# Kernel optimization log

Hardware: AMD Instinct MI355X
Metric: run time of the kernel (lower is better)

## Reference

```python
import jax, jax.numpy as jnp
import numpy as np

H = 50  # hidden_size


def _lstm_layer(x, W_ih, W_hh, b_ih, b_hh):
    """Single LSTM layer, batch_first input x: [B, T, D] -> [B, T, H].
    PyTorch gate order in the 4H dim: i, f, g, o."""
    B, T, D = x.shape
    # Precompute input projections for all timesteps: [T, B, 4H]
    x_proj = jnp.einsum('btd,gd->tbg', x, W_ih) + (b_ih + b_hh)

    def step(carry, xt):
        h, c = carry
        gates = xt + h @ W_hh.T  # [B, 4H]
        i, f, g, o = jnp.split(gates, 4, axis=-1)
        i = jax.nn.sigmoid(i)
        f = jax.nn.sigmoid(f)
        g = jnp.tanh(g)
        o = jax.nn.sigmoid(o)
        c = f * c + i * g
        h = o * jnp.tanh(c)
        return (h, c), h

    h0 = jnp.zeros((B, H), dtype=x.dtype)
    c0 = jnp.zeros((B, H), dtype=x.dtype)
    _, hs = jax.lax.scan(step, (h0, c0), x_proj)  # hs: [T, B, H]
    return jnp.transpose(hs, (1, 0, 2))  # [B, T, H]


def setup_inputs() -> dict:
    key = jax.random.key(0)
    ks = jax.random.split(key, 11)
    B, T = 2048, 512
    s = 1.0 / np.sqrt(H)  # PyTorch uniform init bound
    u = lambda k, shape: jax.random.uniform(k, shape, jnp.float32, -s, s)
    return {
        'x': jax.random.normal(ks[0], (B, T, 1), dtype=jnp.float32),
        'W_ih0': u(ks[1], (4 * H, 1)),
        'W_hh0': u(ks[2], (4 * H, H)),
        'b_ih0': u(ks[3], (4 * H,)),
        'b_hh0': u(ks[4], (4 * H,)),
        'W_ih1': u(ks[5], (4 * H, H)),
        'W_hh1': u(ks[6], (4 * H, H)),
        'b_ih1': u(ks[7], (4 * H,)),
        'b_hh1': u(ks[8], (4 * H,)),
        'W_fc': u(ks[9], (1, H)),
        'b_fc': u(ks[10], (1,)),
    }


def reference(x, W_ih0, W_hh0, b_ih0, b_hh0, W_ih1, W_hh1, b_ih1, b_hh1, W_fc, b_fc):
    out = _lstm_layer(x, W_ih0, W_hh0, b_ih0, b_hh0)     # [B, T, H]
    out = _lstm_layer(out, W_ih1, W_hh1, b_ih1, b_hh1)   # [B, T, H]
    return out[:, -1, :] @ W_fc.T + b_fc                  # [B, 1]
```

## Files before the change

### kernel.cpp

```cpp
#include <hip/hip_runtime.h>

#define TT   512
#define HH   50
#define MB   8
#define NW   13
#define NTHR (NW * 64)

typedef _Float16 f16x8 __attribute__((ext_vector_type(8)));
typedef float    f32x4 __attribute__((ext_vector_type(4)));

#define L2E 1.4426950408889634f

__device__ __forceinline__ float rcp_f(float v) { return __builtin_amdgcn_rcpf(v); }
__device__ __forceinline__ float ex2_f(float v) { return __builtin_amdgcn_exp2f(v); }

__global__ __launch_bounds__(NTHR, 1)
void lstm2_kernel(const float* __restrict__ x,
                  const float* __restrict__ W_ih0, const float* __restrict__ W_hh0,
                  const float* __restrict__ b_ih0, const float* __restrict__ b_hh0,
                  const float* __restrict__ W_ih1, const float* __restrict__ W_hh1,
                  const float* __restrict__ b_ih1, const float* __restrict__ b_hh1,
                  const float* __restrict__ W_fc,  const float* __restrict__ b_fc,
                  float* __restrict__ out)
{
    __shared__ __align__(16) _Float16 sh0[2][2][4][16][8];
    __shared__ __align__(16) _Float16 sh1[2][2][4][16][8];
    __shared__ float sh_x[MB][TT + 4];
    __shared__ float shf[MB][52];
    __shared__ float sh_wfc[HH];

    const int tid = threadIdx.x;
    const int w   = tid >> 6;
    const int l   = tid & 63;
    const int q   = l >> 4;
    const int n   = l & 15;
    const int b0  = blockIdx.x * MB;

    for (int i = tid; i < 2 * 2 * 4 * 16 * 8; i += NTHR) {
        (&sh0[0][0][0][0][0])[i] = (_Float16)0.0f;
        (&sh1[0][0][0][0][0])[i] = (_Float16)0.0f;
    }
    for (int i = tid; i < MB * TT; i += NTHR)
        sh_x[i >> 9][i & (TT - 1)] = x[(size_t)b0 * TT + i];
    for (int i = tid; i < HH; i += NTHR) sh_wfc[i] = W_fc[i];

    const int  u_r   = w * 4 + (n >> 2);
    const bool rowok = (u_r < HH);
    const int  grow  = (n & 3) * HH + (rowok ? u_r : 0);
    const float srow = ((n & 3) == 2) ? (2.0f * L2E) : (-L2E);

    f16x8 whh0[2], wih1[2], whh1[2];
    #pragma unroll
    for (int ki = 0; ki < 2; ++ki) {
        #pragma unroll
        for (int e = 0; e < 8; ++e) {
            int k = ki * 32 + q * 8 + e;
            bool ok = rowok && (k < HH);
            whh0[ki][e] = ok ? (_Float16)(srow * W_hh0[grow * HH + k]) : (_Float16)0.0f;
            wih1[ki][e] = ok ? (_Float16)(srow * W_ih1[grow * HH + k]) : (_Float16)0.0f;
            whh1[ki][e] = ok ? (_Float16)(srow * W_hh1[grow * HH + k]) : (_Float16)0.0f;
        }
    }

    const bool isL1 = (n >= 8);
    const int  u    = 4 * w + q;
    const int  cb   = n & 7;
    const bool wr   = (u < HH);
    const int  uc   = wr ? u : 0;

    float bza[4], wza[4];
    #pragma unroll
    for (int e = 0; e < 4; ++e) {
        int gr = e * HH + uc;
        float sc = (e == 2) ? (2.0f * L2E) : (-L2E);
        bza[e] = sc * (isL1 ? (b_ih1[gr] + b_hh1[gr]) : (b_ih0[gr] + b_hh0[gr]));
        wza[e] = isL1 ? 0.0f : (sc * W_ih0[gr]);
    }

    const int uk = uc >> 5, uq2 = (uc >> 3) & 3, ue = uc & 7;
    _Float16* wpA0 = isL1 ? &sh1[1][uk][uq2][cb + 8][ue] : &sh0[1][uk][uq2][cb][ue];
    _Float16* wpA1 = isL1 ? &sh1[0][uk][uq2][cb + 8][ue] : &sh0[0][uk][uq2][cb][ue];

    const float* xq = &sh_x[cb][0];
    const f32x4 z = {0.0f, 0.0f, 0.0f, 0.0f};
    float cst = 0.0f;

    __syncthreads();

#define MFMA(A, B, C) __builtin_amdgcn_mfma_f32_16x16x32_f16((A), (B), (C), 0, 0, 0)

#define STEP(P, T0, XI)                                                           \
    {                                                                             \
        f16x8 hb0 = *(const f16x8*)&sh0[P][0][q][n][0];                           \
        f16x8 hb1 = *(const f16x8*)&sh0[P][1][q][n][0];                           \
        f16x8 pb0 = *(const f16x8*)&sh1[P][0][q][n][0];                           \
        f16x8 pb1 = *(const f16x8*)&sh1[P][1][q][n][0];                           \
        f32x4 a0 = MFMA(whh0[0], hb0, z);                                         \
        a0 = MFMA(whh0[1], hb1, a0);                                              \
        f32x4 a1 = MFMA(wih1[0], hb0, z);                                         \
        a1 = MFMA(wih1[1], hb1, a1);                                              \
        a1 = MFMA(whh1[0], pb0, a1);                                              \
        a1 = MFMA(whh1[1], pb1, a1);                                              \
        float xi = (XI);                                                          \
        float g0 = (isL1 ? a1[0] : a0[0]) + bza[0];                               \
        float g1 = (isL1 ? a1[1] : a0[1]) + bza[1];                               \
        float g2 = (isL1 ? a1[2] : a0[2]) + bza[2];                               \
        float g3 = (isL1 ? a1[3] : a0[3]) + bza[3];                               \
        g0 = __builtin_fmaf(xi, wza[0], g0);                                      \
        g1 = __builtin_fmaf(xi, wza[1], g1);                                      \
        g2 = __builtin_fmaf(xi, wza[2], g2);                                      \
        g3 = __builtin_fmaf(xi, wza[3], g3);                                      \
        float eI = ex2_f(g0), eF = ex2_f(g1), tG = ex2_f(g2), eO = ex2_f(g3);     \
        float dI = 1.0f + eI, dF = 1.0f + eF, dO = 1.0f + eO;                     \
        float IG = (tG - 1.0f) * rcp_f(dI * (tG + 1.0f));                         \
        float cn = __builtin_fmaf(rcp_f(dF), cst, IG);                            \
        cst = ((T0) && isL1) ? 0.0f : cn;                                         \
        float cc = fminf(fmaxf(cst, -16.0f), 16.0f);                              \
        float tc = ex2_f(cc * (2.0f * L2E));                                      \
        float hv = (tc - 1.0f) * rcp_f(dO * (tc + 1.0f));                         \
        if (wr && !((T0) && isL1)) {                                              \
            _Float16 h16 = (_Float16)hv;                                          \
            _Float16* wp = (P) ? wpA1 : wpA0;                                     \
            wp[0] = h16;                                                          \
            if (!isL1) wp[64] = h16;                     \
        }                                                                         \
        __syncthreads();                                                          \
    }

    STEP(0, 1, xq[0])
    for (int k2 = 0; k2 < 255; ++k2) {
        STEP(1, 0, xq[1])
        STEP(0, 0, xq[2])
        xq += 2;
    }
    STEP(1, 0, xq[1])
#undef STEP

    {
        f16x8 hb0 = *(const f16x8*)&sh0[0][0][q][n][0];
        f16x8 hb1 = *(const f16x8*)&sh0[0][1][q][n][0];
        f16x8 pb0 = *(const f16x8*)&sh1[0][0][q][n][0];
        f16x8 pb1 = *(const f16x8*)&sh1[0][1][q][n][0];
        f32x4 a1 = MFMA(wih1[0], hb0, z);
        a1 = MFMA(wih1[1], hb1, a1);
        a1 = MFMA(whh1[0], pb0, a1);
        a1 = MFMA(whh1[1], pb1, a1);
        if (isL1 && wr) {
            float g0 = a1[0] + bza[0];
            float g1 = a1[1] + bza[1];
            float g2 = a1[2] + bza[2];
            float g3 = a1[3] + bza[3];
            float eI = ex2_f(g0), eF = ex2_f(g1), tG = ex2_f(g2), eO = ex2_f(g3);
            float dI = 1.0f + eI, dF = 1.0f + eF, dO = 1.0f + eO;
            float IG = (tG - 1.0f) * rcp_f(dI * (tG + 1.0f));
            float cn = __builtin_fmaf(rcp_f(dF), cst, IG);
            float cc = fminf(fmaxf(cn, -16.0f), 16.0f);
            float tc = ex2_f(cc * (2.0f * L2E));
            shf[cb][uc] = (tc - 1.0f) * rcp_f(dO * (tc + 1.0f));
        }
    }
    __syncthreads();

    if (tid < MB) {
        float s = b_fc[0];
        for (int j = 0; j < HH; ++j) s += shf[tid][j] * sh_wfc[j];
        out[b0 + tid] = s;
    }
#undef MFMA
}

extern "C" void kernel_launch(void* const* d_in, const int* in_sizes, int n_in,
                              void* d_out, int out_size, void* d_ws, size_t ws_size,
                              hipStream_t stream) {
    const float* xin   = (const float*)d_in[0];
    const float* W_ih0 = (const float*)d_in[1];
    const float* W_hh0 = (const float*)d_in[2];
    const float* b_ih0 = (const float*)d_in[3];
    const float* b_hh0 = (const float*)d_in[4];
    const float* W_ih1 = (const float*)d_in[5];
    const float* W_hh1 = (const float*)d_in[6];
    const float* b_ih1 = (const float*)d_in[7];
    const float* b_hh1 = (const float*)d_in[8];
    const float* W_fc  = (const float*)d_in[9];
    const float* b_fc  = (const float*)d_in[10];
    float* out = (float*)d_out;

    lstm2_kernel<<<dim3(2048 / MB), dim3(NTHR), 0, stream>>>(
        xin, W_ih0, W_hh0, b_ih0, b_hh0, W_ih1, W_hh1, b_ih1, b_hh1, W_fc, b_fc, out);
}
```

Before: 258.3 us.

## Fold input projection and biases into MFMA via augmented hidden-state columns

Appends the scalar input x_t and a constant 1 as extra K columns of the layer-0 hidden buffer, with the corresponding weight columns holding W_ih0 and the biases. The per-step bias adds and input FMAs therefore disappear from the gate computation. One lane copies the next x value into the shared buffer each step, and x is stored as fp16. Layer-1's two MFMA chains are split into independent accumulators to shorten the dependency chain. The trade-off is lower precision, since x and the biases are now rounded to fp16.

```diff
diff --git a/kernel.cpp b/kernel.cpp
--- a/kernel.cpp
+++ b/kernel.cpp
@@ -25,7 +25,7 @@
 {
     __shared__ __align__(16) _Float16 sh0[2][2][4][16][8];
     __shared__ __align__(16) _Float16 sh1[2][2][4][16][8];
-    __shared__ float sh_x[MB][TT + 4];
+    __shared__ _Float16 sh_xh[MB][TT + 8];
     __shared__ float shf[MB][52];
     __shared__ float sh_wfc[HH];
 
@@ -41,8 +41,13 @@
         (&sh1[0][0][0][0][0])[i] = (_Float16)0.0f;
     }
     for (int i = tid; i < MB * TT; i += NTHR)
-        sh_x[i >> 9][i & (TT - 1)] = x[(size_t)b0 * TT + i];
+        sh_xh[i >> 9][i & (TT - 1)] = (_Float16)x[(size_t)b0 * TT + i];
+    for (int i = tid; i < MB * 8; i += NTHR)
+        sh_xh[i >> 3][TT + (i & 7)] = (_Float16)0.0f;
     for (int i = tid; i < HH; i += NTHR) sh_wfc[i] = W_fc[i];
+    __syncthreads();
+    if (tid < 32) sh0[tid >> 4][1][2][tid & 15][3] = (_Float16)1.0f;
+    if (tid < MB) sh0[0][1][2][tid][2] = (_Float16)x[(size_t)(b0 + tid) * TT];
 
     const int  u_r   = w * 4 + (n >> 2);
     const bool rowok = (u_r < HH);
@@ -55,10 +60,22 @@
         #pragma unroll
         for (int e = 0; e < 8; ++e) {
             int k = ki * 32 + q * 8 + e;
-            bool ok = rowok && (k < HH);
-            whh0[ki][e] = ok ? (_Float16)(srow * W_hh0[grow * HH + k]) : (_Float16)0.0f;
-            wih1[ki][e] = ok ? (_Float16)(srow * W_ih1[grow * HH + k]) : (_Float16)0.0f;
-            whh1[ki][e] = ok ? (_Float16)(srow * W_hh1[grow * HH + k]) : (_Float16)0.0f;
+            float a0v = 0.0f, a1v = 0.0f, a2v = 0.0f;
+            if (rowok) {
+                if (k < HH) {
+                    a0v = W_hh0[grow * HH + k];
+                    a1v = W_ih1[grow * HH + k];
+                    a2v = W_hh1[grow * HH + k];
+                } else if (k == HH) {
+                    a0v = W_ih0[grow];
+                } else if (k == HH + 1) {
+                    a0v = b_ih0[grow] + b_hh0[grow];
+                    a1v = b_ih1[grow] + b_hh1[grow];
+                }
+            }
+            whh0[ki][e] = (_Float16)(srow * a0v);
+            wih1[ki][e] = (_Float16)(srow * a1v);
+            whh1[ki][e] = (_Float16)(srow * a2v);
         }
     }
 
@@ -68,28 +85,21 @@
     const bool wr   = (u < HH);
     const int  uc   = wr ? u : 0;
 
-    float bza[4], wza[4];
-    #pragma unroll
-    for (int e = 0; e < 4; ++e) {
-        int gr = e * HH + uc;
-        float sc = (e == 2) ? (2.0f * L2E) : (-L2E);
-        bza[e] = sc * (isL1 ? (b_ih1[gr] + b_hh1[gr]) : (b_ih0[gr] + b_hh0[gr]));
-        wza[e] = isL1 ? 0.0f : (sc * W_ih0[gr]);
-    }
+    const bool wrel = (w == 12) && (q == 2) && (n < 8);
 
     const int uk = uc >> 5, uq2 = (uc >> 3) & 3, ue = uc & 7;
     _Float16* wpA0 = isL1 ? &sh1[1][uk][uq2][cb + 8][ue] : &sh0[1][uk][uq2][cb][ue];
     _Float16* wpA1 = isL1 ? &sh1[0][uk][uq2][cb + 8][ue] : &sh0[0][uk][uq2][cb][ue];
 
-    const float* xq = &sh_x[cb][0];
     const f32x4 z = {0.0f, 0.0f, 0.0f, 0.0f};
     float cst = 0.0f;
+    int   xt  = 1;
 
     __syncthreads();
 
 #define MFMA(A, B, C) __builtin_amdgcn_mfma_f32_16x16x32_f16((A), (B), (C), 0, 0, 0)
 
-#define STEP(P, T0, XI)                                                           \
+#define STEP(P, T0)                                                               \
     {                                                                             \
         f16x8 hb0 = *(const f16x8*)&sh0[P][0][q][n][0];                           \
         f16x8 hb1 = *(const f16x8*)&sh0[P][1][q][n][0];                           \
@@ -99,17 +109,15 @@
         a0 = MFMA(whh0[1], hb1, a0);                                              \
         f32x4 a1 = MFMA(wih1[0], hb0, z);                                         \
         a1 = MFMA(wih1[1], hb1, a1);                                              \
-        a1 = MFMA(whh1[0], pb0, a1);                                              \
-        a1 = MFMA(whh1[1], pb1, a1);                                              \
-        float xi = (XI);                                                          \
-        float g0 = (isL1 ? a1[0] : a0[0]) + bza[0];                               \
-        float g1 = (isL1 ? a1[1] : a0[1]) + bza[1];                               \
-        float g2 = (isL1 ? a1[2] : a0[2]) + bza[2];                               \
-        float g3 = (isL1 ? a1[3] : a0[3]) + bza[3];                               \
-        g0 = __builtin_fmaf(xi, wza[0], g0);                                      \
-        g1 = __builtin_fmaf(xi, wza[1], g1);                                      \
-        g2 = __builtin_fmaf(xi, wza[2], g2);                                      \
-        g3 = __builtin_fmaf(xi, wza[3], g3);                                      \
+        f32x4 a2 = MFMA(whh1[0], pb0, z);                                         \
+        a2 = MFMA(whh1[1], pb1, a2);                                              \
+        a1 += a2;                                                                 \
+        if (wrel) sh0[(P) ^ 1][1][2][n][2] = sh_xh[n][xt];                        \
+        ++xt;                                                                     \
+        float g0 = isL1 ? a1[0] : a0[0];                                          \
+        float g1 = isL1 ? a1[1] : a0[1];                                          \
+        float g2 = isL1 ? a1[2] : a0[2];                                          \
+        float g3 = isL1 ? a1[3] : a0[3];                                          \
         float eI = ex2_f(g0), eF = ex2_f(g1), tG = ex2_f(g2), eO = ex2_f(g3);     \
         float dI = 1.0f + eI, dF = 1.0f + eF, dO = 1.0f + eO;                     \
         float IG = (tG - 1.0f) * rcp_f(dI * (tG + 1.0f));                         \
@@ -127,13 +135,12 @@
         __syncthreads();                                                          \
     }
 
-    STEP(0, 1, xq[0])
+    STEP(0, 1)
     for (int k2 = 0; k2 < 255; ++k2) {
-        STEP(1, 0, xq[1])
-        STEP(0, 0, xq[2])
-        xq += 2;
+        STEP(1, 0)
+        STEP(0, 0)
     }
-    STEP(1, 0, xq[1])
+    STEP(1, 0)
 #undef STEP
 
     {
@@ -146,11 +153,8 @@
         a1 = MFMA(whh1[0], pb0, a1);
         a1 = MFMA(whh1[1], pb1, a1);
         if (isL1 && wr) {
-            float g0 = a1[0] + bza[0];
-            float g1 = a1[1] + bza[1];
-            float g2 = a1[2] + bza[2];
-            float g3 = a1[3] + bza[3];
-            float eI = ex2_f(g0), eF = ex2_f(g1), tG = ex2_f(g2), eO = ex2_f(g3);
+            float eI = ex2_f(a1[0]), eF = ex2_f(a1[1]);
+            float tG = ex2_f(a1[2]), eO = ex2_f(a1[3]);
             float dI = 1.0f + eI, dF = 1.0f + eF, dO = 1.0f + eO;
             float IG = (tG - 1.0f) * rcp_f(dI * (tG + 1.0f));
             float cn = __builtin_fmaf(rcp_f(dF), cst, IG);
```

Result: slower. 282.2 us (+9.3%).

## Split warps into layer-0 and layer-1 groups with two-phase overlapped schedule

Applied to the files above, without the earlier changes.

Restructures the recurrence so 7 warps own layer 0 and 7 own layer 1. Each timestep is split into two barrier-separated phases, so one group's MFMAs overlap with the other group's gate math. Each warp now handles two row tiles with its own weights, instead of every warp computing both layers with half its lanes idle in the gate math. This adds a second __syncthreads per timestep and raises the warp count to 14. It also changes the fp16 h buffer layout for layer 1.

```diff
diff --git a/kernel.cpp b/kernel.cpp
--- a/kernel.cpp
+++ b/kernel.cpp
@@ -3,7 +3,7 @@
 #define TT   512
 #define HH   50
 #define MB   8
-#define NW   13
+#define NW   14
 #define NTHR (NW * 64)
 
 typedef _Float16 f16x8 __attribute__((ext_vector_type(8)));
@@ -13,6 +13,18 @@
 
 __device__ __forceinline__ float rcp_f(float v) { return __builtin_amdgcn_rcpf(v); }
 __device__ __forceinline__ float ex2_f(float v) { return __builtin_amdgcn_exp2f(v); }
+
+__device__ __forceinline__ float lstm_chain(float g0, float g1, float g2, float g3,
+                                            float& cst) {
+    float eI = ex2_f(g0), eF = ex2_f(g1), tG = ex2_f(g2), eO = ex2_f(g3);
+    float dI = 1.0f + eI, dF = 1.0f + eF, dO = 1.0f + eO;
+    float IG = (tG - 1.0f) * rcp_f(dI * (tG + 1.0f));
+    float cn = __builtin_fmaf(rcp_f(dF), cst, IG);
+    cst = cn;
+    float cc = fminf(fmaxf(cn, -16.0f), 16.0f);
+    float tc = ex2_f(cc * (2.0f * L2E));
+    return (tc - 1.0f) * rcp_f(dO * (tc + 1.0f));
+}
 
 __global__ __launch_bounds__(NTHR, 1)
 void lstm2_kernel(const float* __restrict__ x,
@@ -35,6 +47,8 @@
     const int q   = l >> 4;
     const int n   = l & 15;
     const int b0  = blockIdx.x * MB;
+    const bool isA = (w < 7);
+    const int  wg  = isA ? w : (w - 7);
 
     for (int i = tid; i < 2 * 2 * 4 * 16 * 8; i += NTHR) {
         (&sh0[0][0][0][0][0])[i] = (_Float16)0.0f;
@@ -44,120 +58,152 @@
         sh_x[i >> 9][i & (TT - 1)] = x[(size_t)b0 * TT + i];
     for (int i = tid; i < HH; i += NTHR) sh_wfc[i] = W_fc[i];
 
-    const int  u_r   = w * 4 + (n >> 2);
-    const bool rowok = (u_r < HH);
-    const int  grow  = (n & 3) * HH + (rowok ? u_r : 0);
     const float srow = ((n & 3) == 2) ? (2.0f * L2E) : (-L2E);
-
-    f16x8 whh0[2], wih1[2], whh1[2];
+    f16x8 wfA[2][2], wfB[2][2];
     #pragma unroll
-    for (int ki = 0; ki < 2; ++ki) {
+    for (int tt = 0; tt < 2; ++tt) {
+        int tile = 2 * wg + tt;
+        int ur   = 4 * tile + (n >> 2);
+        bool rok = (ur < HH);
+        int grow = (n & 3) * HH + (rok ? ur : 0);
         #pragma unroll
-        for (int e = 0; e < 8; ++e) {
-            int k = ki * 32 + q * 8 + e;
-            bool ok = rowok && (k < HH);
-            whh0[ki][e] = ok ? (_Float16)(srow * W_hh0[grow * HH + k]) : (_Float16)0.0f;
-            wih1[ki][e] = ok ? (_Float16)(srow * W_ih1[grow * HH + k]) : (_Float16)0.0f;
-            whh1[ki][e] = ok ? (_Float16)(srow * W_hh1[grow * HH + k]) : (_Float16)0.0f;
+        for (int ki = 0; ki < 2; ++ki) {
+            #pragma unroll
+            for (int e = 0; e < 8; ++e) {
+                int k = ki * 32 + q * 8 + e;
+                bool ok = rok && (k < HH);
+                float vA = 0.0f, vB = 0.0f;
+                if (ok) {
+                    if (isA) { vA = W_hh0[grow * HH + k]; }
+                    else     { vA = W_ih1[grow * HH + k]; vB = W_hh1[grow * HH + k]; }
+                }
+                wfA[tt][ki][e] = (_Float16)(srow * vA);
+                wfB[tt][ki][e] = (_Float16)(srow * vB);
+            }
         }
     }
 
-    const bool isL1 = (n >= 8);
-    const int  u    = 4 * w + q;
-    const int  cb   = n & 7;
-    const bool wr   = (u < HH);
-    const int  uc   = wr ? u : 0;
-
-    float bza[4], wza[4];
+    const int  u  = 8 * wg + ((n & 8) ? 4 : 0) + q;
+    const int  cb = n & 7;
+    const bool wr = (u < HH);
+    const int  uc = wr ? u : 0;
+
+    float bz[4], wz[4];
     #pragma unroll
     for (int e = 0; e < 4; ++e) {
         int gr = e * HH + uc;
         float sc = (e == 2) ? (2.0f * L2E) : (-L2E);
-        bza[e] = sc * (isL1 ? (b_ih1[gr] + b_hh1[gr]) : (b_ih0[gr] + b_hh0[gr]));
-        wza[e] = isL1 ? 0.0f : (sc * W_ih0[gr]);
+        bz[e] = sc * (isA ? (b_ih0[gr] + b_hh0[gr]) : (b_ih1[gr] + b_hh1[gr]));
+        wz[e] = isA ? (sc * W_ih0[gr]) : 0.0f;
     }
 
     const int uk = uc >> 5, uq2 = (uc >> 3) & 3, ue = uc & 7;
-    _Float16* wpA0 = isL1 ? &sh1[1][uk][uq2][cb + 8][ue] : &sh0[1][uk][uq2][cb][ue];
-    _Float16* wpA1 = isL1 ? &sh1[0][uk][uq2][cb + 8][ue] : &sh0[0][uk][uq2][cb][ue];
+    _Float16* wpP0 = isA ? &sh0[0][uk][uq2][cb][ue] : &sh1[0][uk][uq2][cb][ue];
+    _Float16* wpP1 = isA ? &sh0[1][uk][uq2][cb][ue] : &sh1[1][uk][uq2][cb][ue];
 
     const float* xq = &sh_x[cb][0];
     const f32x4 z = {0.0f, 0.0f, 0.0f, 0.0f};
+    f32x4 acc0 = z, acc1 = z;
     float cst = 0.0f;
 
     __syncthreads();
 
 #define MFMA(A, B, C) __builtin_amdgcn_mfma_f32_16x16x32_f16((A), (B), (C), 0, 0, 0)
 
-#define STEP(P, T0, XI)                                                           \
+#define PHASE1(P, BG)                                                             \
     {                                                                             \
-        f16x8 hb0 = *(const f16x8*)&sh0[P][0][q][n][0];                           \
-        f16x8 hb1 = *(const f16x8*)&sh0[P][1][q][n][0];                           \
-        f16x8 pb0 = *(const f16x8*)&sh1[P][0][q][n][0];                           \
-        f16x8 pb1 = *(const f16x8*)&sh1[P][1][q][n][0];                           \
-        f32x4 a0 = MFMA(whh0[0], hb0, z);                                         \
-        a0 = MFMA(whh0[1], hb1, a0);                                              \
-        f32x4 a1 = MFMA(wih1[0], hb0, z);                                         \
-        a1 = MFMA(wih1[1], hb1, a1);                                              \
-        a1 = MFMA(whh1[0], pb0, a1);                                              \
-        a1 = MFMA(whh1[1], pb1, a1);                                              \
-        float xi = (XI);                                                          \
-        float g0 = (isL1 ? a1[0] : a0[0]) + bza[0];                               \
-        float g1 = (isL1 ? a1[1] : a0[1]) + bza[1];                               \
-        float g2 = (isL1 ? a1[2] : a0[2]) + bza[2];                               \
-        float g3 = (isL1 ? a1[3] : a0[3]) + bza[3];                               \
-        g0 = __builtin_fmaf(xi, wza[0], g0);                                      \
-        g1 = __builtin_fmaf(xi, wza[1], g1);                                      \
-        g2 = __builtin_fmaf(xi, wza[2], g2);                                      \
-        g3 = __builtin_fmaf(xi, wza[3], g3);                                      \
-        float eI = ex2_f(g0), eF = ex2_f(g1), tG = ex2_f(g2), eO = ex2_f(g3);     \
-        float dI = 1.0f + eI, dF = 1.0f + eF, dO = 1.0f + eO;                     \
-        float IG = (tG - 1.0f) * rcp_f(dI * (tG + 1.0f));                         \
-        float cn = __builtin_fmaf(rcp_f(dF), cst, IG);                            \
-        cst = ((T0) && isL1) ? 0.0f : cn;                                         \
-        float cc = fminf(fmaxf(cst, -16.0f), 16.0f);                              \
-        float tc = ex2_f(cc * (2.0f * L2E));                                      \
-        float hv = (tc - 1.0f) * rcp_f(dO * (tc + 1.0f));                         \
-        if (wr && !((T0) && isL1)) {                                              \
-            _Float16 h16 = (_Float16)hv;                                          \
-            _Float16* wp = (P) ? wpA1 : wpA0;                                     \
-            wp[0] = h16;                                                          \
-            if (!isL1) wp[64] = h16;                     \
+        if (isA) {                                                                \
+            f16x8 hb0 = *(const f16x8*)&sh0[(P) ^ 1][0][q][n][0];                 \
+            f16x8 hb1 = *(const f16x8*)&sh0[(P) ^ 1][1][q][n][0];                 \
+            acc0 = MFMA(wfA[0][0], hb0, z);                                       \
+            acc0 = MFMA(wfA[0][1], hb1, acc0);                                    \
+            acc1 = MFMA(wfA[1][0], hb0, z);                                       \
+            acc1 = MFMA(wfA[1][1], hb1, acc1);                                    \
+        } else if (BG) {                                                          \
+            float g0 = ((n & 8) ? acc1[0] : acc0[0]) + bz[0];                     \
+            float g1 = ((n & 8) ? acc1[1] : acc0[1]) + bz[1];                     \
+            float g2 = ((n & 8) ? acc1[2] : acc0[2]) + bz[2];                     \
+            float g3 = ((n & 8) ? acc1[3] : acc0[3]) + bz[3];                     \
+            float hv = lstm_chain(g0, g1, g2, g3, cst);                           \
+            if (wr) {                                                             \
+                _Float16 h16 = (_Float16)hv;                                      \
+                _Float16* wp = (P) ? wpP1 : wpP0;                                 \
+                wp[0] = h16; wp[64] = h16;                                        \
+            }                                                                     \
         }                                                                         \
         __syncthreads();                                                          \
     }
 
-    STEP(0, 1, xq[0])
+#define PHASE2(P, XI)                                                             \
+    {                                                                             \
+        if (isA) {                                                                \
+            float xi = (XI);                                                      \
+            float g0 = __builtin_fmaf(xi, wz[0], ((n & 8) ? acc1[0] : acc0[0]) + bz[0]); \
+            float g1 = __builtin_fmaf(xi, wz[1], ((n & 8) ? acc1[1] : acc0[1]) + bz[1]); \
+            float g2 = __builtin_fmaf(xi, wz[2], ((n & 8) ? acc1[2] : acc0[2]) + bz[2]); \
+            float g3 = __builtin_fmaf(xi, wz[3], ((n & 8) ? acc1[3] : acc0[3]) + bz[3]); \
+            float hv = lstm_chain(g0, g1, g2, g3, cst);                           \
+            if (wr) {                                                             \
+                _Float16 h16 = (_Float16)hv;                                      \
+                _Float16* wp = (P) ? wpP1 : wpP0;                                 \
+                wp[0] = h16; wp[64] = h16;                                        \
+            }                                                                     \
+        } else {                                                                  \
+            f16x8 hb0 = *(const f16x8*)&sh0[(P) ^ 1][0][q][n][0];                 \
+            f16x8 hb1 = *(const f16x8*)&sh0[(P) ^ 1][1][q][n][0];                 \
+            f16x8 pb0 = *(const f16x8*)&sh1[P][0][q][n][0];                       \
+            f16x8 pb1 = *(const f16x8*)&sh1[P][1][q][n][0];                       \
+            acc0 = MFMA(wfA[0][0], hb0, z);                                       \
+            acc0 = MFMA(wfA[0][1], hb1, acc0);                                    \
+            acc0 = MFMA(wfB[0][0], pb0, acc0);                                    \
+            acc0 = MFMA(wfB[0][1], pb1, acc0);                                    \
+            acc1 = MFMA(wfA[1][0], hb0, z);                                       \
+            acc1 = MFMA(wfA[1][1], hb1, acc1);                                    \
+            acc1 = MFMA(wfB[1][0], pb0, acc1);                                    \
+            acc1 = MFMA(wfB[1][1], pb1, acc1);                                    \
+        }                                                                         \
+        __syncthreads();                                                          \
+    }
+
+    PHASE1(0, 0) PHASE2(0, xq[0])
+    PHASE1(1, 0) PHASE2(1, xq[1])
+
     for (int k2 = 0; k2 < 255; ++k2) {
-        STEP(1, 0, xq[1])
-        STEP(0, 0, xq[2])
+        PHASE1(0, 1) PHASE2(0, xq[2])
+        PHASE1(1, 1) PHASE2(1, xq[3])
         xq += 2;
     }
-    STEP(1, 0, xq[1])
-#undef STEP
-
-    {
-        f16x8 hb0 = *(const f16x8*)&sh0[0][0][q][n][0];
-        f16x8 hb1 = *(const f16x8*)&sh0[0][1][q][n][0];
+#undef PHASE1
+#undef PHASE2
+
+    if (!isA) {
+        float g0 = ((n & 8) ? acc1[0] : acc0[0]) + bz[0];
+        float g1 = ((n & 8) ? acc1[1] : acc0[1]) + bz[1];
+        float g2 = ((n & 8) ? acc1[2] : acc0[2]) + bz[2];
+        float g3 = ((n & 8) ? acc1[3] : acc0[3]) + bz[3];
+        float hv = lstm_chain(g0, g1, g2, g3, cst);
+        if (wr) { _Float16 h16 = (_Float16)hv; wpP0[0] = h16; wpP0[64] = h16; }
+    }
+    __syncthreads();
+    if (!isA) {
+        f16x8 hb0 = *(const f16x8*)&sh0[1][0][q][n][0];
+        f16x8 hb1 = *(const f16x8*)&sh0[1][1][q][n][0];
         f16x8 pb0 = *(const f16x8*)&sh1[0][0][q][n][0];
         f16x8 pb1 = *(const f16x8*)&sh1[0][1][q][n][0];
-        f32x4 a1 = MFMA(wih1[0], hb0, z);
-        a1 = MFMA(wih1[1], hb1, a1);
-        a1 = MFMA(whh1[0], pb0, a1);
-        a1 = MFMA(whh1[1], pb1, a1);
-        if (isL1 && wr) {
-            float g0 = a1[0] + bza[0];
-            float g1 = a1[1] + bza[1];
-            float g2 = a1[2] + bza[2];
-            float g3 = a1[3] + bza[3];
-            float eI = ex2_f(g0), eF = ex2_f(g1), tG = ex2_f(g2), eO = ex2_f(g3);
-            float dI = 1.0f + eI, dF = 1.0f + eF, dO = 1.0f + eO;
-            float IG = (tG - 1.0f) * rcp_f(dI * (tG + 1.0f));
-            float cn = __builtin_fmaf(rcp_f(dF), cst, IG);
-            float cc = fminf(fmaxf(cn, -16.0f), 16.0f);
-            float tc = ex2_f(cc * (2.0f * L2E));
-            shf[cb][uc] = (tc - 1.0f) * rcp_f(dO * (tc + 1.0f));
-        }
+        acc0 = MFMA(wfA[0][0], hb0, z);
+        acc0 = MFMA(wfA[0][1], hb1, acc0);
+        acc0 = MFMA(wfB[0][0], pb0, acc0);
+        acc0 = MFMA(wfB[0][1], pb1, acc0);
+        acc1 = MFMA(wfA[1][0], hb0, z);
+        acc1 = MFMA(wfA[1][1], hb1, acc1);
+        acc1 = MFMA(wfB[1][0], pb0, acc1);
+        acc1 = MFMA(wfB[1][1], pb1, acc1);
+        float g0 = ((n & 8) ? acc1[0] : acc0[0]) + bz[0];
+        float g1 = ((n & 8) ? acc1[1] : acc0[1]) + bz[1];
+        float g2 = ((n & 8) ? acc1[2] : acc0[2]) + bz[2];
+        float g3 = ((n & 8) ? acc1[3] : acc0[3]) + bz[3];
+        float hv = lstm_chain(g0, g1, g2, g3, cst);
+        if (wr) shf[cb][uc] = hv;
     }
     __syncthreads();
 
```

Result: slower. 320.3 us (+24.0%).

## Fuse both LSTM layers into one packed MFMA chain with bias in accumulator

Applied to the files above, without the earlier changes.

Packs W_hh0, W_ih1 and W_hh1 into one K=160 weight fragment so each step runs a single five-MFMA chain over a unified shared h buffer, instead of separate layer-0 and layer-1 chains. The bias and input-projection FMA are folded into the accumulator's initial value, and the clamp uses fmed3. This cuts total MFMA count and select logic per step. In exchange, the dependent MFMA chain for layer 0 gets longer and each step needs one more LDS read.

```diff
diff --git a/kernel.cpp b/kernel.cpp
--- a/kernel.cpp
+++ b/kernel.cpp
@@ -5,6 +5,7 @@
 #define MB   8
 #define NW   13
 #define NTHR (NW * 64)
+#define BUFH 2560
 
 typedef _Float16 f16x8 __attribute__((ext_vector_type(8)));
 typedef float    f32x4 __attribute__((ext_vector_type(4)));
@@ -23,8 +24,7 @@
                   const float* __restrict__ W_fc,  const float* __restrict__ b_fc,
                   float* __restrict__ out)
 {
-    __shared__ __align__(16) _Float16 sh0[2][2][4][16][8];
-    __shared__ __align__(16) _Float16 sh1[2][2][4][16][8];
+    __shared__ __align__(16) _Float16 shh[2][BUFH];
     __shared__ float sh_x[MB][TT + 4];
     __shared__ float shf[MB][52];
     __shared__ float sh_wfc[HH];
@@ -36,10 +36,7 @@
     const int n   = l & 15;
     const int b0  = blockIdx.x * MB;
 
-    for (int i = tid; i < 2 * 2 * 4 * 16 * 8; i += NTHR) {
-        (&sh0[0][0][0][0][0])[i] = (_Float16)0.0f;
-        (&sh1[0][0][0][0][0])[i] = (_Float16)0.0f;
-    }
+    for (int i = tid; i < 2 * BUFH; i += NTHR) (&shh[0][0])[i] = (_Float16)0.0f;
     for (int i = tid; i < MB * TT; i += NTHR)
         sh_x[i >> 9][i & (TT - 1)] = x[(size_t)b0 * TT + i];
     for (int i = tid; i < HH; i += NTHR) sh_wfc[i] = W_fc[i];
@@ -49,16 +46,19 @@
     const int  grow  = (n & 3) * HH + (rowok ? u_r : 0);
     const float srow = ((n & 3) == 2) ? (2.0f * L2E) : (-L2E);
 
-    f16x8 whh0[2], wih1[2], whh1[2];
+    f16x8 wf[5];
     #pragma unroll
-    for (int ki = 0; ki < 2; ++ki) {
+    for (int ki = 0; ki < 5; ++ki) {
         #pragma unroll
         for (int e = 0; e < 8; ++e) {
             int k = ki * 32 + q * 8 + e;
-            bool ok = rowok && (k < HH);
-            whh0[ki][e] = ok ? (_Float16)(srow * W_hh0[grow * HH + k]) : (_Float16)0.0f;
-            wih1[ki][e] = ok ? (_Float16)(srow * W_ih1[grow * HH + k]) : (_Float16)0.0f;
-            whh1[ki][e] = ok ? (_Float16)(srow * W_hh1[grow * HH + k]) : (_Float16)0.0f;
+            float v = 0.0f;
+            if (rowok) {
+                if      (k < HH)           v = W_hh0[grow * HH + k];
+                else if (k < 2 * HH)       v = W_ih1[grow * HH + (k - HH)];
+                else if (k < 3 * HH)       v = W_hh1[grow * HH + (k - 2 * HH)];
+            }
+            wf[ki][e] = (_Float16)(srow * v);
         }
     }
 
@@ -68,21 +68,27 @@
     const bool wr   = (u < HH);
     const int  uc   = wr ? u : 0;
 
-    float bza[4], wza[4];
+    float bz[4], wz[4];
     #pragma unroll
     for (int e = 0; e < 4; ++e) {
         int gr = e * HH + uc;
         float sc = (e == 2) ? (2.0f * L2E) : (-L2E);
-        bza[e] = sc * (isL1 ? (b_ih1[gr] + b_hh1[gr]) : (b_ih0[gr] + b_hh0[gr]));
-        wza[e] = isL1 ? 0.0f : (sc * W_ih0[gr]);
+        bz[e] = sc * (isL1 ? (b_ih1[gr] + b_hh1[gr]) : (b_ih0[gr] + b_hh0[gr]));
+        wz[e] = isL1 ? 0.0f : (sc * W_ih0[gr]);
     }
 
-    const int uk = uc >> 5, uq2 = (uc >> 3) & 3, ue = uc & 7;
-    _Float16* wpA0 = isL1 ? &sh1[1][uk][uq2][cb + 8][ue] : &sh0[1][uk][uq2][cb][ue];
-    _Float16* wpA1 = isL1 ? &sh1[0][uk][uq2][cb + 8][ue] : &sh0[0][uk][uq2][cb][ue];
+    auto offrc = [](int r, int c) {
+        return (r >> 5) * 512 + ((r >> 3) & 3) * 128 + c * 8 + (r & 7);
+    };
+    const _Float16* rb = &shh[0][8 * l];
+    const int oa = isL1 ? offrc(100 + uc, cb + 8) : offrc(uc, cb);
+    const int ob = offrc(50 + uc, cb + 8);
+    _Float16* wpa0 = &shh[1][oa];
+    _Float16* wpa1 = &shh[0][oa];
+    _Float16* wpb0 = &shh[1][ob];
+    _Float16* wpb1 = &shh[0][ob];
 
     const float* xq = &sh_x[cb][0];
-    const f32x4 z = {0.0f, 0.0f, 0.0f, 0.0f};
     float cst = 0.0f;
 
     __syncthreads();
@@ -91,38 +97,34 @@
 
 #define STEP(P, T0, XI)                                                           \
     {                                                                             \
-        f16x8 hb0 = *(const f16x8*)&sh0[P][0][q][n][0];                           \
-        f16x8 hb1 = *(const f16x8*)&sh0[P][1][q][n][0];                           \
-        f16x8 pb0 = *(const f16x8*)&sh1[P][0][q][n][0];                           \
-        f16x8 pb1 = *(const f16x8*)&sh1[P][1][q][n][0];                           \
-        f32x4 a0 = MFMA(whh0[0], hb0, z);                                         \
-        a0 = MFMA(whh0[1], hb1, a0);                                              \
-        f32x4 a1 = MFMA(wih1[0], hb0, z);                                         \
-        a1 = MFMA(wih1[1], hb1, a1);                                              \
-        a1 = MFMA(whh1[0], pb0, a1);                                              \
-        a1 = MFMA(whh1[1], pb1, a1);                                              \
         float xi = (XI);                                                          \
-        float g0 = (isL1 ? a1[0] : a0[0]) + bza[0];                               \
-        float g1 = (isL1 ? a1[1] : a0[1]) + bza[1];                               \
-        float g2 = (isL1 ? a1[2] : a0[2]) + bza[2];                               \
-        float g3 = (isL1 ? a1[3] : a0[3]) + bza[3];                               \
-        g0 = __builtin_fmaf(xi, wza[0], g0);                                      \
-        g1 = __builtin_fmaf(xi, wza[1], g1);                                      \
-        g2 = __builtin_fmaf(xi, wza[2], g2);                                      \
-        g3 = __builtin_fmaf(xi, wza[3], g3);                                      \
-        float eI = ex2_f(g0), eF = ex2_f(g1), tG = ex2_f(g2), eO = ex2_f(g3);     \
+        f32x4 cin;                                                                \
+        cin[0] = __builtin_fmaf(xi, wz[0], bz[0]);                                \
+        cin[1] = __builtin_fmaf(xi, wz[1], bz[1]);                                \
+        cin[2] = __builtin_fmaf(xi, wz[2], bz[2]);                                \
+        cin[3] = __builtin_fmaf(xi, wz[3], bz[3]);                                \
+        f16x8 b0 = *(const f16x8*)(rb + (P) * BUFH);                              \
+        f16x8 b1 = *(const f16x8*)(rb + (P) * BUFH + 512);                        \
+        f16x8 b2 = *(const f16x8*)(rb + (P) * BUFH + 1024);                       \
+        f16x8 b3 = *(const f16x8*)(rb + (P) * BUFH + 1536);                       \
+        f16x8 b4 = *(const f16x8*)(rb + (P) * BUFH + 2048);                       \
+        f32x4 a = MFMA(wf[0], b0, cin);                                           \
+        a = MFMA(wf[1], b1, a);                                                   \
+        a = MFMA(wf[2], b2, a);                                                   \
+        a = MFMA(wf[3], b3, a);                                                   \
+        a = MFMA(wf[4], b4, a);                                                   \
+        float eI = ex2_f(a[0]), eF = ex2_f(a[1]), tG = ex2_f(a[2]), eO = ex2_f(a[3]); \
         float dI = 1.0f + eI, dF = 1.0f + eF, dO = 1.0f + eO;                     \
         float IG = (tG - 1.0f) * rcp_f(dI * (tG + 1.0f));                         \
         float cn = __builtin_fmaf(rcp_f(dF), cst, IG);                            \
         cst = ((T0) && isL1) ? 0.0f : cn;                                         \
-        float cc = fminf(fmaxf(cst, -16.0f), 16.0f);                              \
+        float cc = __builtin_amdgcn_fmed3f(cst, -16.0f, 16.0f);                   \
         float tc = ex2_f(cc * (2.0f * L2E));                                      \
         float hv = (tc - 1.0f) * rcp_f(dO * (tc + 1.0f));                         \
         if (wr && !((T0) && isL1)) {                                              \
             _Float16 h16 = (_Float16)hv;                                          \
-            _Float16* wp = (P) ? wpA1 : wpA0;                                     \
-            wp[0] = h16;                                                          \
-            if (!isL1) wp[64] = h16;                     \
+            *((P) ? wpa1 : wpa0) = h16;                                           \
+            if (!isL1) *((P) ? wpb1 : wpb0) = h16;                                \
         }                                                                         \
         __syncthreads();                                                          \
     }
@@ -137,24 +139,23 @@
 #undef STEP
 
     {
-        f16x8 hb0 = *(const f16x8*)&sh0[0][0][q][n][0];
-        f16x8 hb1 = *(const f16x8*)&sh0[0][1][q][n][0];
-        f16x8 pb0 = *(const f16x8*)&sh1[0][0][q][n][0];
-        f16x8 pb1 = *(const f16x8*)&sh1[0][1][q][n][0];
-        f32x4 a1 = MFMA(wih1[0], hb0, z);
-        a1 = MFMA(wih1[1], hb1, a1);
-        a1 = MFMA(whh1[0], pb0, a1);
-        a1 = MFMA(whh1[1], pb1, a1);
+        f32x4 cin = {bz[0], bz[1], bz[2], bz[3]};
+        f16x8 b0 = *(const f16x8*)(rb);
+        f16x8 b1 = *(const f16x8*)(rb + 512);
+        f16x8 b2 = *(const f16x8*)(rb + 1024);
+        f16x8 b3 = *(const f16x8*)(rb + 1536);
+        f16x8 b4 = *(const f16x8*)(rb + 2048);
+        f32x4 a = MFMA(wf[0], b0, cin);
+        a = MFMA(wf[1], b1, a);
+        a = MFMA(wf[2], b2, a);
+        a = MFMA(wf[3], b3, a);
+        a = MFMA(wf[4], b4, a);
         if (isL1 && wr) {
-            float g0 = a1[0] + bza[0];
-            float g1 = a1[1] + bza[1];
-            float g2 = a1[2] + bza[2];
-            float g3 = a1[3] + bza[3];
-            float eI = ex2_f(g0), eF = ex2_f(g1), tG = ex2_f(g2), eO = ex2_f(g3);
+            float eI = ex2_f(a[0]), eF = ex2_f(a[1]), tG = ex2_f(a[2]), eO = ex2_f(a[3]);
             float dI = 1.0f + eI, dF = 1.0f + eF, dO = 1.0f + eO;
             float IG = (tG - 1.0f) * rcp_f(dI * (tG + 1.0f));
             float cn = __builtin_fmaf(rcp_f(dF), cst, IG);
-            float cc = fminf(fmaxf(cn, -16.0f), 16.0f);
+            float cc = __builtin_amdgcn_fmed3f(cn, -16.0f, 16.0f);
             float tc = ex2_f(cc * (2.0f * L2E));
             shf[cb][uc] = (tc - 1.0f) * rcp_f(dO * (tc + 1.0f));
         }
```

Result: faster. 240.6 us, median of 2 (-6.8%).
